# Optimization experiments

Hardware: AMD Instinct MI355X
Metric: run time of the kernel (lower is better)

Reference implementation:

```python
import jax, jax.numpy as jnp
import numpy as np
import math

B, SQ, SKV = 8, 1024, 1024
D, H, DQ, DV = 1024, 16, 64, 64
EPS = 1e-3  # Keras LayerNormalization default epsilon
IN_DECODER = True


def _layer_norm(x, gamma, beta):
    m = jnp.mean(x, axis=-1, keepdims=True)
    v = jnp.mean((x - m) ** 2, axis=-1, keepdims=True)
    return gamma * (x - m) / jnp.sqrt(v + EPS) + beta


def setup_inputs() -> dict:
    key = jax.random.key(0)
    ks = jax.random.split(key, 6)
    x = jax.random.normal(ks[0], (B, SQ, D), dtype=jnp.float32)
    # self-attention: query and key/value sequences are the same tensor
    lengths = jax.random.randint(ks[1], (B,), SKV // 2, SKV + 1, dtype=jnp.int32)
    init = 0.02
    Wq = jax.random.normal(ks[2], (D, H * DQ), dtype=jnp.float32) * init
    Wkv = jax.random.normal(ks[3], (D, H * (DQ + DV)), dtype=jnp.float32) * init
    Wo = jax.random.normal(ks[4], (H * DV, D), dtype=jnp.float32) * init
    return {
        "query_sequences": x,
        "key_value_sequences": x,
        "key_value_sequence_lengths": lengths,
        "Wq": Wq, "bq": jnp.zeros((H * DQ,), jnp.float32),
        "Wkv": Wkv, "bkv": jnp.zeros((H * (DQ + DV),), jnp.float32),
        "Wo": Wo, "bo": jnp.zeros((D,), jnp.float32),
        "ln_gamma": jnp.ones((D,), jnp.float32),
        "ln_beta": jnp.zeros((D,), jnp.float32),
    }


def reference(query_sequences, key_value_sequences, key_value_sequence_lengths,
              Wq, bq, Wkv, bkv, Wo, bo, ln_gamma, ln_beta):
    # detect self-attention exactly as the original (elementwise equality)
    self_attn = jnp.all(query_sequences == key_value_sequences)
    q_seq = _layer_norm(query_sequences, ln_gamma, ln_beta)
    kv_ln = _layer_norm(key_value_sequences, ln_gamma, ln_beta)
    kv_seq = jnp.where(self_attn, kv_ln, key_value_sequences)
    residual = q_seq  # pre-norm residual (original adds post-LN queries)

    q = (q_seq @ Wq + bq).reshape(B, SQ, H, DQ).transpose(0, 2, 1, 3)   # b h q d
    kvp = kv_seq @ Wkv + bkv
    k = kvp[..., : H * DQ].reshape(B, SKV, H, DQ).transpose(0, 2, 1, 3)  # b h k d
    v = kvp[..., H * DQ:].reshape(B, SKV, H, DV).transpose(0, 2, 1, 3)   # b h k d

    scores = jnp.einsum("bhqd,bhkd->bhqk", q, k) / math.sqrt(DQ)
    # padding mask on keys
    not_pad = (jnp.arange(SKV)[None, None, None, :]
               < key_value_sequence_lengths[:, None, None, None])
    scores = jnp.where(not_pad, scores, -jnp.inf)
    if IN_DECODER:
        causal = jnp.tril(jnp.ones((SQ, SKV), dtype=bool))[None, None]
        scores = jnp.where(jnp.logical_or(~self_attn, causal), scores, -jnp.inf)

    attn = jax.nn.softmax(scores, axis=-1)  # dropout is identity in eval mode
    out = jnp.einsum("bhqk,bhkd->bhqd", attn, v)
    out = out.transpose(0, 2, 1, 3).reshape(B, SQ, H * DV)
    out = out @ Wo + bo
    return out + residual
```

## Files before the change

### kernel.cpp

```cpp
#include <hip/hip_runtime.h>

typedef unsigned short u16;
typedef unsigned int u32;
typedef __attribute__((ext_vector_type(8))) short short8;
typedef __attribute__((ext_vector_type(4))) float fx4;

#define LOG2E 1.44269504088896340736f

__device__ __forceinline__ u16 f2bf(float f) {
    unsigned int u = __float_as_uint(f);
    u += 0x7fffu + ((u >> 16) & 1u);
    return (u16)(u >> 16);
}

__device__ __forceinline__ float bf2f(u16 v) {
    u32 u = ((u32)v) << 16;
    return __uint_as_float(u);
}

__device__ __forceinline__ u32 pack_bf2(float lo, float hi) {
    return __builtin_amdgcn_perm(__float_as_uint(hi), __float_as_uint(lo), 0x07060302u);
}

__device__ __forceinline__ float fast_exp2(float x) {
#if __has_builtin(__builtin_amdgcn_exp2f)
    return __builtin_amdgcn_exp2f(x);
#else
    return exp2f(x);
#endif
}

__device__ __forceinline__ fx4 mfma16(short8 a, short8 b, fx4 c) {
    return __builtin_amdgcn_mfma_f32_16x16x32_bf16(a, b, c, 0, 0, 0);
}

__device__ __forceinline__ void gload_lds16(const u16* g, u16* l) {
    __builtin_amdgcn_global_load_lds(
        (const __attribute__((address_space(1))) void*)g,
        (__attribute__((address_space(3))) void*)l, 16, 0, 0);
}

__global__ __launch_bounds__(256) void ln_kernel(
    const float* __restrict__ x, const float* __restrict__ gamma,
    const float* __restrict__ beta, u16* __restrict__ yb) {
    int row = blockIdx.x;
    int t = threadIdx.x;
    const float* xr = x + ((size_t)row << 10);
    float4 v = *(const float4*)(xr + (t << 2));
    float s  = v.x + v.y + v.z + v.w;
    float sq = v.x * v.x + v.y * v.y + v.z * v.z + v.w * v.w;
#pragma unroll
    for (int o = 32; o > 0; o >>= 1) {
        s  += __shfl_down(s, o, 64);
        sq += __shfl_down(sq, o, 64);
    }
    __shared__ float red[8];
    int wv = t >> 6, ln = t & 63;
    if (ln == 0) { red[wv] = s; red[4 + wv] = sq; }
    __syncthreads();
    s  = red[0] + red[1] + red[2] + red[3];
    sq = red[4] + red[5] + red[6] + red[7];
    float mean = s * (1.0f / 1024.0f);
    float var  = sq * (1.0f / 1024.0f) - mean * mean;
    float rstd = rsqrtf(var + 1e-3f);
    float4 g  = *(const float4*)(gamma + (t << 2));
    float4 bb = *(const float4*)(beta + (t << 2));
    float4 y;
    y.x = (v.x - mean) * rstd * g.x + bb.x;
    y.y = (v.y - mean) * rstd * g.y + bb.y;
    y.z = (v.z - mean) * rstd * g.z + bb.z;
    y.w = (v.w - mean) * rstd * g.w + bb.w;
    unsigned long long p = (unsigned long long)f2bf(y.x)
        | ((unsigned long long)f2bf(y.y) << 16)
        | ((unsigned long long)f2bf(y.z) << 32)
        | ((unsigned long long)f2bf(y.w) << 48);
    *(unsigned long long*)(yb + ((size_t)row << 10) + (t << 2)) = p;
}

__global__ __launch_bounds__(256) void wt_kernel(
    const float* __restrict__ W, u16* __restrict__ Wt, int K, int N) {
    __shared__ float tile[32][33];
    int n0 = blockIdx.x << 5, k0 = blockIdx.y << 5;
    int tx = threadIdx.x & 31, ty = threadIdx.x >> 5;
#pragma unroll
    for (int r = 0; r < 4; ++r)
        tile[ty + r * 8][tx] = W[(size_t)(k0 + ty + r * 8) * N + n0 + tx];
    __syncthreads();
#pragma unroll
    for (int r = 0; r < 4; ++r)
        Wt[(size_t)(n0 + ty + r * 8) * K + k0 + tx] = f2bf(tile[tx][ty + r * 8]);
}

__global__ __launch_bounds__(256) void vtrans_kernel(
    const u16* __restrict__ KVp, u16* __restrict__ Vt) {
    int bh = blockIdx.x;
    int b = bh >> 4, h = bh & 15;
    int kt = blockIdx.y;
    int t = threadIdx.x;
    __shared__ u16 tile[64][80];
    int seg = t & 7;
#pragma unroll
    for (int p = 0; p < 2; ++p) {
        int k = (t >> 3) + (p << 5);
        *(uint4*)&tile[k][seg << 3] =
            *(const uint4*)(KVp + (size_t)((b << 10) + (kt << 6) + k) * 2048
                            + 1024 + (h << 6) + (seg << 3));
    }
    __syncthreads();
#pragma unroll
    for (int p = 0; p < 2; ++p) {
        int d = (t >> 3) + (p << 5);
        __align__(16) u16 vals[8];
#pragma unroll
        for (int e = 0; e < 8; ++e) {
            int kp = (seg << 3) + e;
            int ksrc = ((kp & 3) << 4) + (kp >> 2);
            vals[e] = tile[ksrc][d];
        }
        *(uint4*)(Vt + (size_t)((bh << 6) + d) * 1024 + (kt << 6) + (seg << 3)) =
            *(uint4*)vals;
    }
}

template <int MODE>
__global__ __launch_bounds__(256) void gemm_bt(
    const u16* __restrict__ A, const u16* __restrict__ Bt,
    const float* __restrict__ bias, const u16* __restrict__ resb,
    float* __restrict__ Cf, u16* __restrict__ Cb, int M, int N, int K,
    float scale) {
    __shared__ __align__(16) u16 sA[128 * 64];
    __shared__ __align__(16) u16 sB[128 * 64];
    int m0 = blockIdx.y << 7, n0 = blockIdx.x << 7;
    int tid = threadIdx.x, lane = tid & 63, wave = tid >> 6;
    int quad = lane >> 4, l15 = lane & 15, swr = lane & 7;
    int wm = (wave >> 1) << 6, wn = (wave & 1) << 6;
    int srow = lane >> 3;
    int gseg = (lane & 7) ^ srow;

    fx4 acc[4][4];
    fx4 zero = {0.0f, 0.0f, 0.0f, 0.0f};
#pragma unroll
    for (int i = 0; i < 4; ++i)
#pragma unroll
        for (int j = 0; j < 4; ++j) acc[i][j] = zero;

    for (int k0 = 0; k0 < K; k0 += 64) {
#pragma unroll
        for (int t = 0; t < 4; ++t) {
            int c = (wave << 2) + t;
            int row = (c << 3) + srow;
            gload_lds16(A + (size_t)(m0 + row) * K + k0 + (gseg << 3), &sA[c << 9]);
            gload_lds16(Bt + (size_t)(n0 + row) * K + k0 + (gseg << 3), &sB[c << 9]);
        }
        __syncthreads();
#pragma unroll
        for (int kk = 0; kk < 64; kk += 32) {
            int ks = (kk >> 3) + quad;
            short8 af[4], bf[4];
#pragma unroll
            for (int mt = 0; mt < 4; ++mt) {
                int r = wm + (mt << 4) + l15;
                af[mt] = *(const short8*)&sA[(r << 6) + (((ks ^ swr) & 7) << 3)];
            }
#pragma unroll
            for (int nt = 0; nt < 4; ++nt) {
                int r = wn + (nt << 4) + l15;
                bf[nt] = *(const short8*)&sB[(r << 6) + (((ks ^ swr) & 7) << 3)];
            }
#pragma unroll
            for (int mt = 0; mt < 4; ++mt)
#pragma unroll
                for (int nt = 0; nt < 4; ++nt)
                    acc[mt][nt] = mfma16(af[mt], bf[nt], acc[mt][nt]);
        }
        __syncthreads();
    }

#pragma unroll
    for (int mt = 0; mt < 4; ++mt)
#pragma unroll
        for (int nt = 0; nt < 4; ++nt)
#pragma unroll
            for (int r = 0; r < 4; ++r) {
                int row = m0 + wm + (mt << 4) + (quad << 2) + r;
                int col = n0 + wn + (nt << 4) + l15;
                float v = (acc[mt][nt][r] + bias[col]) * scale;
                if (MODE == 1) {
                    size_t idx = (size_t)row * N + col;
                    Cf[idx] = v + bf2f(resb[idx]);
                } else {
                    Cb[(size_t)row * N + col] = f2bf(v);
                }
            }
}

__global__ __launch_bounds__(256) void attn_kernel(
    const u16* __restrict__ Q, const u16* __restrict__ KV,
    const u16* __restrict__ Vt, const int* __restrict__ lens,
    u16* __restrict__ O) {
    int bh = blockIdx.x;
    int b = bh >> 4, h = bh & 15;
    int j = blockIdx.y;
    int len = lens[b];
    int cap = (len - 1) >> 6;
    int tid = threadIdx.x, lane = tid & 63, w = tid >> 6;
    int quad = lane >> 4, l15 = lane & 15;

    __shared__ __align__(16) u16 sK[64 * 64];
    __shared__ __align__(16) u16 sV[64 * 64];
    __shared__ __align__(16) u16 sP[4 * 2048];
    u16* sPw = &sP[w << 11];

    int lrow = lane >> 3;
    int lseg = lane & 7;

    fx4 zero = {0.0f, 0.0f, 0.0f, 0.0f};

#pragma unroll
    for (int phase = 0; phase < 2; ++phase) {
        int s = phase ? (7 - j) : j;
        int q0 = s << 7;
        int wq0 = q0 + (w << 5);
        int ktend_blk = min((q0 + 127) >> 6, cap);
        int ktend_w   = min((wq0 + 31) >> 6, cap);

        short8 qf[2][2];
#pragma unroll
        for (int mt = 0; mt < 2; ++mt)
#pragma unroll
            for (int kk = 0; kk < 2; ++kk) {
                int qrow = (b << 10) + wq0 + (mt << 4) + l15;
                qf[mt][kk] = *(const short8*)(Q + ((size_t)qrow << 10)
                              + (h << 6) + (kk << 5) + (quad << 3));
            }

        fx4 oacc[2][4];
        float lsum[2][4];
#pragma unroll
        for (int mt = 0; mt < 2; ++mt)
#pragma unroll
            for (int nt = 0; nt < 4; ++nt) oacc[mt][nt] = zero;
#pragma unroll
        for (int mt = 0; mt < 2; ++mt)
#pragma unroll
            for (int r = 0; r < 4; ++r) lsum[mt][r] = 0.0f;

        for (int kt = 0; kt <= ktend_blk; ++kt) {
            int k0g = kt << 6;
#pragma unroll
            for (int i = 0; i < 2; ++i) {
                int row = (w << 4) + (i << 3) + lrow;
                int gs = lseg ^ (row & 7);
                gload_lds16(KV + (size_t)((b << 10) + k0g + row) * 2048
                               + (h << 6) + (gs << 3),
                            &sK[((w << 1) + i) << 9]);
                gload_lds16(Vt + (size_t)((bh << 6) + row) * 1024
                               + k0g + (gs << 3),
                            &sV[((w << 1) + i) << 9]);
            }
            __syncthreads();

            if (kt <= ktend_w) {
                fx4 sacc[2][4];
#pragma unroll
                for (int mt = 0; mt < 2; ++mt)
#pragma unroll
                    for (int nt = 0; nt < 4; ++nt) sacc[mt][nt] = zero;
#pragma unroll
                for (int kk = 0; kk < 2; ++kk) {
                    int seg = (kk << 2) + quad;
                    short8 kf[4];
#pragma unroll
                    for (int nt = 0; nt < 4; ++nt) {
                        int row = (nt << 4) + l15;
                        kf[nt] = *(const short8*)&sK[(row << 6)
                                   + (((seg ^ (row & 7)) & 7) << 3)];
                    }
#pragma unroll
                    for (int mt = 0; mt < 2; ++mt)
#pragma unroll
                        for (int nt = 0; nt < 4; ++nt)
                            sacc[mt][nt] = mfma16(qf[mt][kk], kf[nt], sacc[mt][nt]);
                }

                bool needm = ((k0g + 63) > wq0) || ((k0g + 64) > len);
                if (needm) {
#pragma unroll
                    for (int mt = 0; mt < 2; ++mt)
#pragma unroll
                        for (int nt = 0; nt < 4; ++nt) {
                            int kg = k0g + (nt << 4) + l15;
#pragma unroll
                            for (int r = 0; r < 4; ++r) {
                                int qr = wq0 + (mt << 4) + (quad << 2) + r;
                                if (kg > qr || kg >= len)
                                    sacc[mt][nt][r] = -30000.0f;
                            }
                        }
                }

#pragma unroll
                for (int mt = 0; mt < 2; ++mt) {
#pragma unroll
                    for (int nt = 0; nt < 4; ++nt)
#pragma unroll
                        for (int r = 0; r < 4; ++r)
                            sacc[mt][nt][r] = fast_exp2(sacc[mt][nt][r]);
#pragma unroll
                    for (int r = 0; r < 4; ++r) {
                        lsum[mt][r] += (sacc[mt][0][r] + sacc[mt][1][r])
                                     + (sacc[mt][2][r] + sacc[mt][3][r]);
                        int row = (mt << 4) + (quad << 2) + r;
                        u32 lo = pack_bf2(sacc[mt][0][r], sacc[mt][1][r]);
                        u32 hi = pack_bf2(sacc[mt][2][r], sacc[mt][3][r]);
                        uint2 pv; pv.x = lo; pv.y = hi;
                        int addr = (row << 6)
                                 + (((((l15 >> 1)) ^ (row & 7)) & 7) << 3)
                                 + ((l15 & 1) << 2);
                        *(uint2*)&sPw[addr] = pv;
                    }
                }
                __builtin_amdgcn_s_waitcnt(0xC07F);

#pragma unroll
                for (int kk = 0; kk < 2; ++kk) {
                    int seg = (kk << 2) + quad;
                    short8 vf[4], pf[2];
#pragma unroll
                    for (int nt = 0; nt < 4; ++nt) {
                        int row = (nt << 4) + l15;
                        vf[nt] = *(const short8*)&sV[(row << 6)
                                   + (((seg ^ (row & 7)) & 7) << 3)];
                    }
#pragma unroll
                    for (int mt = 0; mt < 2; ++mt) {
                        int row = (mt << 4) + l15;
                        pf[mt] = *(const short8*)&sPw[(row << 6)
                                   + (((seg ^ (row & 7)) & 7) << 3)];
                    }
#pragma unroll
                    for (int mt = 0; mt < 2; ++mt)
#pragma unroll
                        for (int nt = 0; nt < 4; ++nt)
                            oacc[mt][nt] = mfma16(pf[mt], vf[nt], oacc[mt][nt]);
                }
            }
            __syncthreads();
        }

#pragma unroll
        for (int mt = 0; mt < 2; ++mt)
#pragma unroll
            for (int r = 0; r < 4; ++r) {
                float v = lsum[mt][r];
                v += __shfl_xor(v, 1, 64);
                v += __shfl_xor(v, 2, 64);
                v += __shfl_xor(v, 4, 64);
                v += __shfl_xor(v, 8, 64);
                lsum[mt][r] = __builtin_amdgcn_rcpf(v);
            }
#pragma unroll
        for (int mt = 0; mt < 2; ++mt)
#pragma unroll
            for (int nt = 0; nt < 4; ++nt)
#pragma unroll
                for (int r = 0; r < 4; ++r) {
                    int row = (b << 10) + wq0 + (mt << 4) + (quad << 2) + r;
                    int col = (h << 6) + (nt << 4) + l15;
                    O[((size_t)row << 10) + col] =
                        f2bf(oacc[mt][nt][r] * lsum[mt][r]);
                }
    }
}

extern "C" void kernel_launch(void* const* d_in, const int* in_sizes, int n_in,
                              void* d_out, int out_size, void* d_ws, size_t ws_size,
                              hipStream_t stream) {
    (void)in_sizes; (void)n_in; (void)out_size; (void)ws_size;
    const float* x    = (const float*)d_in[0];
    const int*   lens = (const int*)d_in[2];
    const float* Wq   = (const float*)d_in[3];
    const float* bq   = (const float*)d_in[4];
    const float* Wkv  = (const float*)d_in[5];
    const float* bkv  = (const float*)d_in[6];
    const float* Wo   = (const float*)d_in[7];
    const float* bo   = (const float*)d_in[8];
    const float* gam  = (const float*)d_in[9];
    const float* bet  = (const float*)d_in[10];
    float* out = (float*)d_out;

    char* w = (char*)d_ws;
    u16* xln_b = (u16*)w;  w += (size_t)8192 * 1024 * 2;
    u16* Wq_t  = (u16*)w;  w += (size_t)1024 * 1024 * 2;
    u16* Wkv_t = (u16*)w;  w += (size_t)2048 * 1024 * 2;
    u16* Wo_t  = (u16*)w;  w += (size_t)1024 * 1024 * 2;
    u16* Qp    = (u16*)w;  w += (size_t)8192 * 1024 * 2;
    u16* KVp   = (u16*)w;  w += (size_t)8192 * 2048 * 2;
    u16* Vt    = (u16*)w;  w += (size_t)8192 * 1024 * 2;
    u16* AO    = (u16*)w;  w += (size_t)8192 * 1024 * 2;

    ln_kernel<<<8192, 256, 0, stream>>>(x, gam, bet, xln_b);
    wt_kernel<<<dim3(32, 32), 256, 0, stream>>>(Wq, Wq_t, 1024, 1024);
    wt_kernel<<<dim3(64, 32), 256, 0, stream>>>(Wkv, Wkv_t, 1024, 2048);
    wt_kernel<<<dim3(32, 32), 256, 0, stream>>>(Wo, Wo_t, 1024, 1024);
    gemm_bt<0><<<dim3(8, 64), 256, 0, stream>>>(xln_b, Wq_t, bq, nullptr,
        nullptr, Qp, 8192, 1024, 1024, 0.125f * LOG2E);
    gemm_bt<0><<<dim3(16, 64), 256, 0, stream>>>(xln_b, Wkv_t, bkv, nullptr,
        nullptr, KVp, 8192, 2048, 1024, 1.0f);
    vtrans_kernel<<<dim3(128, 16), 256, 0, stream>>>(KVp, Vt);
    attn_kernel<<<dim3(128, 4), 256, 0, stream>>>(Qp, KVp, Vt, lens, AO);
    gemm_bt<1><<<dim3(8, 64), 256, 0, stream>>>(AO, Wo_t, bo, xln_b,
        out, nullptr, 8192, 1024, 1024, 1.0f);
}
```

Before: 278.1 us.

## Fuse Q and KV projections into one GEMM and merge weight transposes

Concatenates the Q and KV projection weights so a single GEMM with N=3072 produces a combined QKV buffer. The epilogue picks the bias per column and applies the softmax scale only to the Q columns, and the attention and V-transpose kernels index into the strided combined buffer. The three weight-transpose launches become one, and layer norm now handles four rows per block with wave-level shuffles instead of a shared-memory reduction. This removes launches and gives the GEMM a larger grid, at the cost of per-element branches in the epilogue and wider row strides for the Q/K loads.

Result: faster. 268.4 us (-3.5%).

```diff
diff --git a/kernel.cpp b/kernel.cpp
--- a/kernel.cpp
+++ b/kernel.cpp
@@ -43,56 +43,67 @@
 __global__ __launch_bounds__(256) void ln_kernel(
     const float* __restrict__ x, const float* __restrict__ gamma,
     const float* __restrict__ beta, u16* __restrict__ yb) {
-    int row = blockIdx.x;
-    int t = threadIdx.x;
+    int wave = threadIdx.x >> 6, lane = threadIdx.x & 63;
+    int row = (blockIdx.x << 2) + wave;
     const float* xr = x + ((size_t)row << 10);
-    float4 v = *(const float4*)(xr + (t << 2));
-    float s  = v.x + v.y + v.z + v.w;
-    float sq = v.x * v.x + v.y * v.y + v.z * v.z + v.w * v.w;
+    float4 v[4];
+    float s = 0.0f, sq = 0.0f;
+#pragma unroll
+    for (int i = 0; i < 4; ++i) {
+        v[i] = *(const float4*)(xr + (i << 8) + (lane << 2));
+        s  += v[i].x + v[i].y + v[i].z + v[i].w;
+        sq += v[i].x * v[i].x + v[i].y * v[i].y + v[i].z * v[i].z + v[i].w * v[i].w;
+    }
 #pragma unroll
     for (int o = 32; o > 0; o >>= 1) {
-        s  += __shfl_down(s, o, 64);
-        sq += __shfl_down(sq, o, 64);
-    }
-    __shared__ float red[8];
-    int wv = t >> 6, ln = t & 63;
-    if (ln == 0) { red[wv] = s; red[4 + wv] = sq; }
-    __syncthreads();
-    s  = red[0] + red[1] + red[2] + red[3];
-    sq = red[4] + red[5] + red[6] + red[7];
+        s  += __shfl_xor(s, o, 64);
+        sq += __shfl_xor(sq, o, 64);
+    }
     float mean = s * (1.0f / 1024.0f);
     float var  = sq * (1.0f / 1024.0f) - mean * mean;
     float rstd = rsqrtf(var + 1e-3f);
-    float4 g  = *(const float4*)(gamma + (t << 2));
-    float4 bb = *(const float4*)(beta + (t << 2));
-    float4 y;
-    y.x = (v.x - mean) * rstd * g.x + bb.x;
-    y.y = (v.y - mean) * rstd * g.y + bb.y;
-    y.z = (v.z - mean) * rstd * g.z + bb.z;
-    y.w = (v.w - mean) * rstd * g.w + bb.w;
-    unsigned long long p = (unsigned long long)f2bf(y.x)
-        | ((unsigned long long)f2bf(y.y) << 16)
-        | ((unsigned long long)f2bf(y.z) << 32)
-        | ((unsigned long long)f2bf(y.w) << 48);
-    *(unsigned long long*)(yb + ((size_t)row << 10) + (t << 2)) = p;
+#pragma unroll
+    for (int i = 0; i < 4; ++i) {
+        int off = (i << 8) + (lane << 2);
+        float4 g  = *(const float4*)(gamma + off);
+        float4 bb = *(const float4*)(beta + off);
+        float4 y;
+        y.x = (v[i].x - mean) * rstd * g.x + bb.x;
+        y.y = (v[i].y - mean) * rstd * g.y + bb.y;
+        y.z = (v[i].z - mean) * rstd * g.z + bb.z;
+        y.w = (v[i].w - mean) * rstd * g.w + bb.w;
+        u32 lo = pack_bf2(y.x, y.y) ;
+        unsigned long long p = (unsigned long long)f2bf(y.x)
+            | ((unsigned long long)f2bf(y.y) << 16)
+            | ((unsigned long long)f2bf(y.z) << 32)
+            | ((unsigned long long)f2bf(y.w) << 48);
+        (void)lo;
+        *(unsigned long long*)(yb + ((size_t)row << 10) + off) = p;
+    }
 }
 
 __global__ __launch_bounds__(256) void wt_kernel(
-    const float* __restrict__ W, u16* __restrict__ Wt, int K, int N) {
+    const float* __restrict__ Wq, const float* __restrict__ Wkv,
+    const float* __restrict__ Wo, u16* __restrict__ Wt) {
+    int n0 = blockIdx.x << 5;
+    int k0 = blockIdx.y << 5;
+    const float* W; int sn0, SN;
+    if (n0 < 1024)      { W = Wq;  sn0 = n0;        SN = 1024; }
+    else if (n0 < 3072) { W = Wkv; sn0 = n0 - 1024; SN = 2048; }
+    else                { W = Wo;  sn0 = n0 - 3072; SN = 1024; }
     __shared__ float tile[32][33];
-    int n0 = blockIdx.x << 5, k0 = blockIdx.y << 5;
     int tx = threadIdx.x & 31, ty = threadIdx.x >> 5;
 #pragma unroll
     for (int r = 0; r < 4; ++r)
-        tile[ty + r * 8][tx] = W[(size_t)(k0 + ty + r * 8) * N + n0 + tx];
+        tile[ty + r * 8][tx] = W[(size_t)(k0 + ty + r * 8) * SN + sn0 + tx];
     __syncthreads();
 #pragma unroll
     for (int r = 0; r < 4; ++r)
-        Wt[(size_t)(n0 + ty + r * 8) * K + k0 + tx] = f2bf(tile[tx][ty + r * 8]);
+        Wt[(size_t)(n0 + ty + r * 8) * 1024 + k0 + tx] = f2bf(tile[tx][ty + r * 8]);
 }
 
 __global__ __launch_bounds__(256) void vtrans_kernel(
-    const u16* __restrict__ KVp, u16* __restrict__ Vt) {
+    const u16* __restrict__ QKVp, u16* __restrict__ Vt) {
     int bh = blockIdx.x;
     int b = bh >> 4, h = bh & 15;
     int kt = blockIdx.y;
@@ -103,8 +114,8 @@
     for (int p = 0; p < 2; ++p) {
         int k = (t >> 3) + (p << 5);
         *(uint4*)&tile[k][seg << 3] =
-            *(const uint4*)(KVp + (size_t)((b << 10) + (kt << 6) + k) * 2048
-                            + 1024 + (h << 6) + (seg << 3));
+            *(const uint4*)(QKVp + (size_t)((b << 10) + (kt << 6) + k) * 3072
+                            + 2048 + (h << 6) + (seg << 3));
     }
     __syncthreads();
 #pragma unroll
@@ -125,9 +136,9 @@
 template <int MODE>
 __global__ __launch_bounds__(256) void gemm_bt(
     const u16* __restrict__ A, const u16* __restrict__ Bt,
-    const float* __restrict__ bias, const u16* __restrict__ resb,
-    float* __restrict__ Cf, u16* __restrict__ Cb, int M, int N, int K,
-    float scale) {
+    const float* __restrict__ bq, const float* __restrict__ bkv,
+    const u16* __restrict__ resb, float* __restrict__ Cf, u16* __restrict__ Cb,
+    int M, int N, int K, float qscale) {
     __shared__ __align__(16) u16 sA[128 * 64];
     __shared__ __align__(16) u16 sB[128 * 64];
     int m0 = blockIdx.y << 7, n0 = blockIdx.x << 7;
@@ -184,20 +195,22 @@
             for (int r = 0; r < 4; ++r) {
                 int row = m0 + wm + (mt << 4) + (quad << 2) + r;
                 int col = n0 + wn + (nt << 4) + l15;
-                float v = (acc[mt][nt][r] + bias[col]) * scale;
                 if (MODE == 1) {
+                    float v = acc[mt][nt][r] + bq[col];
                     size_t idx = (size_t)row * N + col;
                     Cf[idx] = v + bf2f(resb[idx]);
                 } else {
+                    float bias = (col < 1024) ? bq[col] : bkv[col - 1024];
+                    float v = acc[mt][nt][r] + bias;
+                    if (col < 1024) v *= qscale;
                     Cb[(size_t)row * N + col] = f2bf(v);
                 }
             }
 }
 
 __global__ __launch_bounds__(256) void attn_kernel(
-    const u16* __restrict__ Q, const u16* __restrict__ KV,
-    const u16* __restrict__ Vt, const int* __restrict__ lens,
-    u16* __restrict__ O) {
+    const u16* __restrict__ QKVp, const u16* __restrict__ Vt,
+    const int* __restrict__ lens, u16* __restrict__ O) {
     int bh = blockIdx.x;
     int b = bh >> 4, h = bh & 15;
     int j = blockIdx.y;
@@ -230,7 +243,7 @@
 #pragma unroll
             for (int kk = 0; kk < 2; ++kk) {
                 int qrow = (b << 10) + wq0 + (mt << 4) + l15;
-                qf[mt][kk] = *(const short8*)(Q + ((size_t)qrow << 10)
+                qf[mt][kk] = *(const short8*)(QKVp + (size_t)qrow * 3072
                               + (h << 6) + (kk << 5) + (quad << 3));
             }
 
@@ -251,8 +264,8 @@
             for (int i = 0; i < 2; ++i) {
                 int row = (w << 4) + (i << 3) + lrow;
                 int gs = lseg ^ (row & 7);
-                gload_lds16(KV + (size_t)((b << 10) + k0g + row) * 2048
-                               + (h << 6) + (gs << 3),
+                gload_lds16(QKVp + (size_t)((b << 10) + k0g + row) * 3072
+                               + 1024 + (h << 6) + (gs << 3),
                             &sK[((w << 1) + i) << 9]);
                 gload_lds16(Vt + (size_t)((bh << 6) + row) * 1024
                                + k0g + (gs << 3),
@@ -390,25 +403,18 @@
     float* out = (float*)d_out;
 
     char* w = (char*)d_ws;
-    u16* xln_b = (u16*)w;  w += (size_t)8192 * 1024 * 2;
-    u16* Wq_t  = (u16*)w;  w += (size_t)1024 * 1024 * 2;
-    u16* Wkv_t = (u16*)w;  w += (size_t)2048 * 1024 * 2;
-    u16* Wo_t  = (u16*)w;  w += (size_t)1024 * 1024 * 2;
-    u16* Qp    = (u16*)w;  w += (size_t)8192 * 1024 * 2;
-    u16* KVp   = (u16*)w;  w += (size_t)8192 * 2048 * 2;
-    u16* Vt    = (u16*)w;  w += (size_t)8192 * 1024 * 2;
-    u16* AO    = (u16*)w;  w += (size_t)8192 * 1024 * 2;
-
-    ln_kernel<<<8192, 256, 0, stream>>>(x, gam, bet, xln_b);
-    wt_kernel<<<dim3(32, 32), 256, 0, stream>>>(Wq, Wq_t, 1024, 1024);
-    wt_kernel<<<dim3(64, 32), 256, 0, stream>>>(Wkv, Wkv_t, 1024, 2048);
-    wt_kernel<<<dim3(32, 32), 256, 0, stream>>>(Wo, Wo_t, 1024, 1024);
-    gemm_bt<0><<<dim3(8, 64), 256, 0, stream>>>(xln_b, Wq_t, bq, nullptr,
-        nullptr, Qp, 8192, 1024, 1024, 0.125f * LOG2E);
-    gemm_bt<0><<<dim3(16, 64), 256, 0, stream>>>(xln_b, Wkv_t, bkv, nullptr,
-        nullptr, KVp, 8192, 2048, 1024, 1.0f);
-    vtrans_kernel<<<dim3(128, 16), 256, 0, stream>>>(KVp, Vt);
-    attn_kernel<<<dim3(128, 4), 256, 0, stream>>>(Qp, KVp, Vt, lens, AO);
-    gemm_bt<1><<<dim3(8, 64), 256, 0, stream>>>(AO, Wo_t, bo, xln_b,
-        out, nullptr, 8192, 1024, 1024, 1.0f);
-}
+    u16* xln_b  = (u16*)w;  w += (size_t)8192 * 1024 * 2;
+    u16* Wall_t = (u16*)w;  w += (size_t)4096 * 1024 * 2;
+    u16* QKVp   = (u16*)w;  w += (size_t)8192 * 3072 * 2;
+    u16* Vt     = (u16*)w;  w += (size_t)8192 * 1024 * 2;
+    u16* AO     = (u16*)w;  w += (size_t)8192 * 1024 * 2;
+
+    ln_kernel<<<2048, 256, 0, stream>>>(x, gam, bet, xln_b);
+    wt_kernel<<<dim3(128, 32), 256, 0, stream>>>(Wq, Wkv, Wo, Wall_t);
+    gemm_bt<0><<<dim3(24, 64), 256, 0, stream>>>(xln_b, Wall_t, bq, bkv,
+        nullptr, nullptr, QKVp, 8192, 3072, 1024, 0.125f * LOG2E);
+    vtrans_kernel<<<dim3(128, 16), 256, 0, stream>>>(QKVp, Vt);
+    attn_kernel<<<dim3(128, 4), 256, 0, stream>>>(QKVp, Vt, lens, AO);
+    gemm_bt<1><<<dim3(8, 64), 256, 0, stream>>>(AO, Wall_t + (size_t)3072 * 1024,
+        bo, nullptr, xln_b, out, nullptr, 8192, 1024, 1024, 1.0f);
+}
```
